# Performance work log

Hardware: AMD Instinct MI355X
Metric: run time of the kernel (lower is better)

Reference implementation:

```python
import jax, jax.numpy as jnp
import numpy as np

D_MODEL = 1024
N_HEADS = 16
D_K = D_MODEL // N_HEADS
B, T = 2, 2048
EPS = 1e-6


def _phi(x):
    # elu(x) + 1
    return jax.nn.elu(x) + 1.0


def setup_inputs() -> dict:
    key = jax.random.key(0)
    ks = jax.random.split(key, 5)
    s = 1.0 / np.sqrt(D_MODEL)
    return {
        "x": jax.random.normal(ks[0], (B, T, D_MODEL), jnp.float32),
        "Wq": jax.random.normal(ks[1], (D_MODEL, D_MODEL), jnp.float32) * s,
        "bq": jnp.zeros((D_MODEL,), jnp.float32),
        "Wk": jax.random.normal(ks[2], (D_MODEL, D_MODEL), jnp.float32) * s,
        "bk": jnp.zeros((D_MODEL,), jnp.float32),
        "Wv": jax.random.normal(ks[3], (D_MODEL, D_MODEL), jnp.float32) * s,
        "bv": jnp.zeros((D_MODEL,), jnp.float32),
        "Wo": jax.random.normal(ks[4], (D_MODEL, D_MODEL), jnp.float32) * s,
        "bo": jnp.zeros((D_MODEL,), jnp.float32),
    }


def reference(x, Wq, bq, Wk, bk, Wv, bv, Wo, bo):
    Bv_, Tv_, _ = x.shape
    # projections (torch nn.Linear: x @ W.T + b), split heads -> [B, H, T, d_k]
    def proj(W, b):
        y = x @ W.T + b
        return y.reshape(Bv_, Tv_, N_HEADS, D_K).transpose(0, 2, 1, 3)

    q = _phi(proj(Wq, bq))
    k = _phi(proj(Wk, bk))
    v = proj(Wv, bv)

    # causal linear attention: running kv outer-product and k prefix sums
    kv = jnp.einsum("bhtd,bhte->bhtde", k, v)          # [B,H,T,d_k,d_k]
    kv = jnp.cumsum(kv, axis=2)
    k_cum = jnp.cumsum(k, axis=2)
    out = jnp.einsum("bhtd,bhtde->bhte", q, kv)        # [B,H,T,d_k]
    z = jnp.einsum("bhtd,bhtd->bht", q, k_cum)         # [B,H,T]
    out = out / (z[..., None] + EPS)

    out = out.transpose(0, 2, 1, 3).reshape(Bv_, Tv_, N_HEADS * D_K)
    return out @ Wo.T + bo
```

## Files before the change

kernel.cpp:

```cpp
#include <hip/hip_runtime.h>


typedef float  f32x4   __attribute__((ext_vector_type(4)));
typedef __bf16 bf16x8  __attribute__((ext_vector_type(8)));
typedef short  short8v __attribute__((ext_vector_type(8)));
typedef short  short4v __attribute__((ext_vector_type(4)));

static __device__ __forceinline__ short f2bf(float f) {
    unsigned u = __float_as_uint(f);
    u += 0x7FFFu + ((u >> 16) & 1u);
    return (short)(u >> 16);
}
static __device__ __forceinline__ float bf2f(short s) {
    return __uint_as_float(((unsigned)(unsigned short)s) << 16);
}
static __device__ __forceinline__ float phi(float x) {
    return x > 0.f ? x + 1.f : __expf(x);
}
static __device__ __forceinline__ void gl_lds16(const short* g, short* l) {
    __builtin_amdgcn_global_load_lds(
        (const __attribute__((address_space(1))) void*)g,
        (__attribute__((address_space(3))) void*)l, 16, 0, 0);
}

#define LDT 72

__global__ __launch_bounds__(256) void convert_bf16(
    const float* __restrict__ x,  const float* __restrict__ Wq,
    const float* __restrict__ Wk, const float* __restrict__ Wv,
    const float* __restrict__ Wo,
    short* __restrict__ xb,  short* __restrict__ Wqb,
    short* __restrict__ Wkb, short* __restrict__ Wvb, short* __restrict__ Wob)
{
    const int blk = blockIdx.x;
    const float* src; short* dst; size_t base;
    if (blk < 2048)      { src = x;  dst = xb;  base = (size_t)blk * 2048; }
    else if (blk < 2560) { src = Wq; dst = Wqb; base = (size_t)(blk - 2048) * 2048; }
    else if (blk < 3072) { src = Wk; dst = Wkb; base = (size_t)(blk - 2560) * 2048; }
    else if (blk < 3584) { src = Wv; dst = Wvb; base = (size_t)(blk - 3072) * 2048; }
    else                 { src = Wo; dst = Wob; base = (size_t)(blk - 3584) * 2048; }
    const size_t o = base + (size_t)threadIdx.x * 8;
    f32x4 v0 = *(const f32x4*)&src[o];
    f32x4 v1 = *(const f32x4*)&src[o + 4];
    short8v s;
#pragma unroll
    for (int m = 0; m < 4; ++m) { s[m] = f2bf(v0[m]); s[m + 4] = f2bf(v1[m]); }
    *(short8v*)&dst[o] = s;
}

__global__ __launch_bounds__(256) void gemm_qkv(
    const short* __restrict__ xb,
    const short* __restrict__ Wqb, const short* __restrict__ Wkb,
    const short* __restrict__ Wvb,
    const float* __restrict__ bq, const float* __restrict__ bk,
    const float* __restrict__ bv,
    short* __restrict__ Qb, short* __restrict__ Kb, short* __restrict__ Vb)
{
    __shared__ short As[128 * 32];
    __shared__ short Bs[128 * 32];
    const int tid = threadIdx.x;
    const int bm = blockIdx.x, bn = blockIdx.y;
    const int wsel = bn >> 3;
    const int n0 = (bn & 7) << 7;
    const short* __restrict__ W    = (wsel == 0) ? Wqb : (wsel == 1) ? Wkb : Wvb;
    const float* __restrict__ bias = (wsel == 0) ? bq  : (wsel == 1) ? bk  : bv;
    short* __restrict__ Ob         = (wsel == 0) ? Qb  : (wsel == 1) ? Kb  : Vb;
    const int m0 = bm << 7;
    const int wave = tid >> 6, lane = tid & 63;
    const int wm = (wave & 1) << 6, wn = (wave >> 1) << 6;
    const int l15 = lane & 15, quad = lane >> 4;

    const int ch0 = wave * 2, ch1 = ch0 + 1;
    const int lrow = lane >> 2, lcol = (lane & 3) << 3;
    const short* ga0 = xb + (size_t)(m0 + ch0 * 16 + lrow) * 1024 + lcol;
    const short* ga1 = xb + (size_t)(m0 + ch1 * 16 + lrow) * 1024 + lcol;
    const short* gb0 = W  + (size_t)(n0 + ch0 * 16 + lrow) * 1024 + lcol;
    const short* gb1 = W  + (size_t)(n0 + ch1 * 16 + lrow) * 1024 + lcol;
    short* la0 = &As[ch0 * 512];
    short* la1 = &As[ch1 * 512];
    short* lb0 = &Bs[ch0 * 512];
    short* lb1 = &Bs[ch1 * 512];

    f32x4 acc[4][4] = {};
    for (int k0 = 0; k0 < 1024; k0 += 32) {
        __syncthreads();
        gl_lds16(ga0 + k0, la0);
        gl_lds16(ga1 + k0, la1);
        gl_lds16(gb0 + k0, lb0);
        gl_lds16(gb1 + k0, lb1);
        __syncthreads();
        bf16x8 a[4], b[4];
#pragma unroll
        for (int i = 0; i < 4; ++i) a[i] = *(const bf16x8*)&As[(wm + i * 16 + l15) * 32 + quad * 8];
#pragma unroll
        for (int j = 0; j < 4; ++j) b[j] = *(const bf16x8*)&Bs[(wn + j * 16 + l15) * 32 + quad * 8];
#pragma unroll
        for (int i = 0; i < 4; ++i)
#pragma unroll
            for (int j = 0; j < 4; ++j)
                acc[i][j] = __builtin_amdgcn_mfma_f32_16x16x32_bf16(a[i], b[j], acc[i][j], 0, 0, 0);
    }

#pragma unroll
    for (int i = 0; i < 4; ++i)
#pragma unroll
        for (int j = 0; j < 4; ++j) {
            const int col = n0 + wn + j * 16 + l15;
            const float bv_ = bias[col];
#pragma unroll
            for (int r = 0; r < 4; ++r) {
                const int row = m0 + wm + i * 16 + quad * 4 + r;
                float v = acc[i][j][r] + bv_;
                if (wsel < 2) v = phi(v);
                Ob[(size_t)row * 1024 + col] = f2bf(v);
            }
        }
}

__global__ __launch_bounds__(256) void chunk_sums(
    const short* __restrict__ Kb, const short* __restrict__ Vb,
    short* __restrict__ KVsum, float* __restrict__ ksum)
{
    __shared__ short KT[64 * LDT];
    __shared__ short VT[64 * LDT];
    __shared__ float pS[256];
    const int c = blockIdx.x, bh = blockIdx.y;
    const int b = bh >> 4, h = bh & 15;
    const int tid = threadIdx.x;
    const int w = tid >> 6, lane = tid & 63, l15 = lane & 15, quad = lane >> 4;
    const size_t rowbase = (size_t)b * 2048 + c * 64;

#pragma unroll
    for (int p = 0; p < 2; ++p) {
        const int t = (tid >> 3) + p * 32;
        const int e0 = (tid & 7) << 3;
        const size_t g = (rowbase + t) * 1024 + h * 64 + e0;
        short8v kv = *(const short8v*)&Kb[g];
        short8v vv = *(const short8v*)&Vb[g];
#pragma unroll
        for (int jj = 0; jj < 8; ++jj) {
            KT[(e0 + jj) * LDT + t] = kv[jj];
            VT[(e0 + jj) * LDT + t] = vv[jj];
        }
    }
    __syncthreads();

    f32x4 acc[4] = {};
#pragma unroll
    for (int k0 = 0; k0 < 64; k0 += 32) {
        bf16x8 a = *(const bf16x8*)&KT[(w * 16 + l15) * LDT + k0 + quad * 8];
#pragma unroll
        for (int tj = 0; tj < 4; ++tj) {
            bf16x8 bfr = *(const bf16x8*)&VT[(tj * 16 + l15) * LDT + k0 + quad * 8];
            acc[tj] = __builtin_amdgcn_mfma_f32_16x16x32_bf16(a, bfr, acc[tj], 0, 0, 0);
        }
    }
    short* __restrict__ outp = KVsum + (((size_t)bh * 32) + c) * 4096;
#pragma unroll
    for (int tj = 0; tj < 4; ++tj)
#pragma unroll
        for (int r = 0; r < 4; ++r)
            outp[(w * 16 + quad * 4 + r) * 64 + tj * 16 + l15] = f2bf(acc[tj][r]);

    {
        const int d = tid & 63, part = tid >> 6;
        short8v k1 = *(const short8v*)&KT[d * LDT + part * 16];
        short8v k2 = *(const short8v*)&KT[d * LDT + part * 16 + 8];
        float s = 0.f;
#pragma unroll
        for (int m = 0; m < 8; ++m) s += bf2f(k1[m]) + bf2f(k2[m]);
        pS[part * 64 + d] = s;
    }
    __syncthreads();
    if (tid < 64)
        ksum[(((size_t)bh * 32) + c) * 64 + tid] =
            pS[tid] + pS[tid + 64] + pS[tid + 128] + pS[tid + 192];
}

__global__ __launch_bounds__(256) void scan_chunks(
    const short* __restrict__ KVsum, const float* __restrict__ ksum,
    short* __restrict__ KVpref, float* __restrict__ kpref)
{
    const int bh = blockIdx.y;
    const int o = blockIdx.x * 256 + threadIdx.x;
    float run = 0.f;
    size_t base = (size_t)bh * 32 * 4096 + o;
    for (int cc = 0; cc < 32; ++cc) {
        KVpref[base] = f2bf(run);
        run += bf2f(KVsum[base]);
        base += 4096;
    }
    if (blockIdx.x == 0 && threadIdx.x < 64) {
        float vals[32];
        const size_t kb = (size_t)bh * 32 * 64 + threadIdx.x;
#pragma unroll
        for (int cc = 0; cc < 32; ++cc) vals[cc] = ksum[kb + (size_t)cc * 64];
        float r2 = 0.f;
#pragma unroll
        for (int cc = 0; cc < 32; ++cc) { kpref[kb + (size_t)cc * 64] = r2; r2 += vals[cc]; }
    }
}

__global__ __launch_bounds__(256) void attn_chunk(
    const short* __restrict__ Qb, const short* __restrict__ Kb,
    const short* __restrict__ Vb, const short* __restrict__ KVpref,
    const float* __restrict__ kpref, short* __restrict__ attnb)
{
    __shared__ short Qs[64 * LDT];
    __shared__ short KS[64 * LDT];
    __shared__ short VT[64 * LDT];
    __shared__ short KVT[64 * LDT];
    const int c = blockIdx.x, bh = blockIdx.y;
    const int b = bh >> 4, h = bh & 15;
    const int tid = threadIdx.x;
    const int w = tid >> 6, lane = tid & 63, l15 = lane & 15, quad = lane >> 4;
    const size_t rowbase = (size_t)b * 2048 + c * 64;
    const short* __restrict__ KVc = KVpref + (((size_t)bh * 32) + c) * 4096;

#pragma unroll
    for (int p = 0; p < 2; ++p) {
        const int t = (tid >> 3) + p * 32;
        const int e0 = (tid & 7) << 3;
        const size_t g = (rowbase + t) * 1024 + h * 64 + e0;
        *(short8v*)&Qs[t * LDT + e0] = *(const short8v*)&Qb[g];
        *(short8v*)&KS[t * LDT + e0] = *(const short8v*)&Kb[g];
        short8v vv = *(const short8v*)&Vb[g];
        short8v pv = *(const short8v*)&KVc[t * 64 + e0];
#pragma unroll
        for (int jj = 0; jj < 8; ++jj) {
            VT[(e0 + jj) * LDT + t]  = vv[jj];
            KVT[(e0 + jj) * LDT + t] = pv[jj];
        }
    }
    __syncthreads();

    f32x4 sacc[4] = {};
#pragma unroll
    for (int k0 = 0; k0 < 64; k0 += 32) {
        bf16x8 a = *(const bf16x8*)&Qs[(w * 16 + l15) * LDT + k0 + quad * 8];
#pragma unroll
        for (int tj = 0; tj < 4; ++tj) {
            bf16x8 bfr = *(const bf16x8*)&KS[(tj * 16 + l15) * LDT + k0 + quad * 8];
            sacc[tj] = __builtin_amdgcn_mfma_f32_16x16x32_bf16(a, bfr, sacc[tj], 0, 0, 0);
        }
    }

    f32x4 kp4 = *(const f32x4*)&kpref[(((size_t)bh * 32) + c) * 64 + l15 * 4];
    float zinv[4];
#pragma unroll
    for (int r = 0; r < 4; ++r) {
        const int i = w * 16 + quad * 4 + r;
        float p = 0.f;
#pragma unroll
        for (int tj = 0; tj < 4; ++tj)
            if (tj * 16 + l15 <= i) p += sacc[tj][r];
        short4v q4 = *(const short4v*)&Qs[i * LDT + l15 * 4];
#pragma unroll
        for (int m = 0; m < 4; ++m) p += bf2f(q4[m]) * kp4[m];
        p += __shfl_xor(p, 1);
        p += __shfl_xor(p, 2);
        p += __shfl_xor(p, 4);
        p += __shfl_xor(p, 8);
        zinv[r] = 1.f / (p + 1e-6f);
    }

    __syncthreads();
#pragma unroll
    for (int tj = 0; tj < 4; ++tj)
#pragma unroll
        for (int r = 0; r < 4; ++r) {
            const int i = w * 16 + quad * 4 + r;
            const int j = tj * 16 + l15;
            KS[i * LDT + j] = f2bf(j <= i ? sacc[tj][r] : 0.f);
        }
    __syncthreads();

    f32x4 oacc[4] = {};
#pragma unroll
    for (int k0 = 0; k0 < 64; k0 += 32) {
        bf16x8 a1 = *(const bf16x8*)&KS[(w * 16 + l15) * LDT + k0 + quad * 8];
        bf16x8 a2 = *(const bf16x8*)&Qs[(w * 16 + l15) * LDT + k0 + quad * 8];
#pragma unroll
        for (int tj = 0; tj < 4; ++tj) {
            bf16x8 b1 = *(const bf16x8*)&VT[(tj * 16 + l15) * LDT + k0 + quad * 8];
            bf16x8 b2 = *(const bf16x8*)&KVT[(tj * 16 + l15) * LDT + k0 + quad * 8];
            oacc[tj] = __builtin_amdgcn_mfma_f32_16x16x32_bf16(a1, b1, oacc[tj], 0, 0, 0);
            oacc[tj] = __builtin_amdgcn_mfma_f32_16x16x32_bf16(a2, b2, oacc[tj], 0, 0, 0);
        }
    }
#pragma unroll
    for (int tj = 0; tj < 4; ++tj)
#pragma unroll
        for (int r = 0; r < 4; ++r) {
            const int i = w * 16 + quad * 4 + r;
            const int e = tj * 16 + l15;
            attnb[(rowbase + i) * 1024 + h * 64 + e] = f2bf(oacc[tj][r] * zinv[r]);
        }
}

__global__ __launch_bounds__(256) void gemm_out(
    const short* __restrict__ attnb, const short* __restrict__ Wob,
    const float* __restrict__ bo, float* __restrict__ outp)
{
    __shared__ short As[128 * 32];
    __shared__ short Bs[128 * 32];
    const int tid = threadIdx.x;
    const int bm = blockIdx.x, bn = blockIdx.y;
    const int m0 = bm << 7, n0 = bn << 7;
    const int wave = tid >> 6, lane = tid & 63;
    const int wm = (wave & 1) << 6, wn = (wave >> 1) << 6;
    const int l15 = lane & 15, quad = lane >> 4;

    const int ch0 = wave * 2, ch1 = ch0 + 1;
    const int lrow = lane >> 2, lcol = (lane & 3) << 3;
    const short* ga0 = attnb + (size_t)(m0 + ch0 * 16 + lrow) * 1024 + lcol;
    const short* ga1 = attnb + (size_t)(m0 + ch1 * 16 + lrow) * 1024 + lcol;
    const short* gb0 = Wob   + (size_t)(n0 + ch0 * 16 + lrow) * 1024 + lcol;
    const short* gb1 = Wob   + (size_t)(n0 + ch1 * 16 + lrow) * 1024 + lcol;
    short* la0 = &As[ch0 * 512];
    short* la1 = &As[ch1 * 512];
    short* lb0 = &Bs[ch0 * 512];
    short* lb1 = &Bs[ch1 * 512];

    f32x4 acc[4][4] = {};
    for (int k0 = 0; k0 < 1024; k0 += 32) {
        __syncthreads();
        gl_lds16(ga0 + k0, la0);
        gl_lds16(ga1 + k0, la1);
        gl_lds16(gb0 + k0, lb0);
        gl_lds16(gb1 + k0, lb1);
        __syncthreads();
        bf16x8 a[4], b[4];
#pragma unroll
        for (int i = 0; i < 4; ++i) a[i] = *(const bf16x8*)&As[(wm + i * 16 + l15) * 32 + quad * 8];
#pragma unroll
        for (int j = 0; j < 4; ++j) b[j] = *(const bf16x8*)&Bs[(wn + j * 16 + l15) * 32 + quad * 8];
#pragma unroll
        for (int i = 0; i < 4; ++i)
#pragma unroll
            for (int j = 0; j < 4; ++j)
                acc[i][j] = __builtin_amdgcn_mfma_f32_16x16x32_bf16(a[i], b[j], acc[i][j], 0, 0, 0);
    }

#pragma unroll
    for (int i = 0; i < 4; ++i)
#pragma unroll
        for (int j = 0; j < 4; ++j) {
            const int col = n0 + wn + j * 16 + l15;
            const float bv_ = bo[col];
#pragma unroll
            for (int r = 0; r < 4; ++r) {
                const int row = m0 + wm + i * 16 + quad * 4 + r;
                outp[(size_t)row * 1024 + col] = acc[i][j][r] + bv_;
            }
        }
}

extern "C" void kernel_launch(void* const* d_in, const int* in_sizes, int n_in,
                              void* d_out, int out_size, void* d_ws, size_t ws_size,
                              hipStream_t stream)
{
    const float* x  = (const float*)d_in[0];
    const float* Wq = (const float*)d_in[1];
    const float* bq = (const float*)d_in[2];
    const float* Wk = (const float*)d_in[3];
    const float* bk = (const float*)d_in[4];
    const float* Wv = (const float*)d_in[5];
    const float* bv = (const float*)d_in[6];
    const float* Wo = (const float*)d_in[7];
    const float* bo = (const float*)d_in[8];

    char* ws = (char*)d_ws;
    short* xb     = (short*)(ws + 0);
    short* Wqb    = (short*)(ws + 8388608);
    short* Wkb    = (short*)(ws + 10485760);
    short* Wvb    = (short*)(ws + 12582912);
    short* Wob    = (short*)(ws + 14680064);
    short* Qb     = (short*)(ws + 16777216);
    short* Kb     = (short*)(ws + 25165824);
    short* Vb     = (short*)(ws + 33554432);
    short* KVsum  = (short*)(ws + 41943040);
    short* attnb  = (short*)(ws + 41943040);
    short* KVpref = (short*)(ws + 50331648);
    float* ksum   = (float*)(ws + 58720256);
    float* kpref  = (float*)(ws + 58982400);
    float* outp   = (float*)d_out;

    convert_bf16<<<4096, 256, 0, stream>>>(x, Wq, Wk, Wv, Wo, xb, Wqb, Wkb, Wvb, Wob);
    gemm_qkv   <<<dim3(32, 24), 256, 0, stream>>>(xb, Wqb, Wkb, Wvb, bq, bk, bv, Qb, Kb, Vb);
    chunk_sums <<<dim3(32, 32), 256, 0, stream>>>(Kb, Vb, KVsum, ksum);
    scan_chunks<<<dim3(16, 32), 256, 0, stream>>>(KVsum, ksum, KVpref, kpref);
    attn_chunk <<<dim3(32, 32), 256, 0, stream>>>(Qb, Kb, Vb, KVpref, kpref, attnb);
    gemm_out   <<<dim3(32, 8), 256, 0, stream>>>(attnb, Wob, bo, outp);
}
```

Measured before the change: 169.2 us.

## Fuse chunk prefix scan into attention kernel and shrink output GEMM N-tile

Removes the separate scan_chunks kernel. Each attention block now sums the preceding chunks' KV and k sums itself, in float registers, before writing the prefix into shared memory. This saves a kernel launch and the KVpref round trip through memory. In exchange, the redundant reads are quadratic in chunk index, so later chunks load up to 31 chunk-sums each. Separately, the output GEMM tile goes from 128x128 to 128x64, doubling the block count to 512 for better CU occupancy at the cost of more A-tile reloads.

```diff
diff --git a/kernel.cpp b/kernel.cpp
--- a/kernel.cpp
+++ b/kernel.cpp
@@ -177,59 +177,58 @@
             pS[tid] + pS[tid + 64] + pS[tid + 128] + pS[tid + 192];
 }
 
-__global__ __launch_bounds__(256) void scan_chunks(
-    const short* __restrict__ KVsum, const float* __restrict__ ksum,
-    short* __restrict__ KVpref, float* __restrict__ kpref)
-{
-    const int bh = blockIdx.y;
-    const int o = blockIdx.x * 256 + threadIdx.x;
-    float run = 0.f;
-    size_t base = (size_t)bh * 32 * 4096 + o;
-    for (int cc = 0; cc < 32; ++cc) {
-        KVpref[base] = f2bf(run);
-        run += bf2f(KVsum[base]);
-        base += 4096;
-    }
-    if (blockIdx.x == 0 && threadIdx.x < 64) {
-        float vals[32];
-        const size_t kb = (size_t)bh * 32 * 64 + threadIdx.x;
-#pragma unroll
-        for (int cc = 0; cc < 32; ++cc) vals[cc] = ksum[kb + (size_t)cc * 64];
-        float r2 = 0.f;
-#pragma unroll
-        for (int cc = 0; cc < 32; ++cc) { kpref[kb + (size_t)cc * 64] = r2; r2 += vals[cc]; }
-    }
-}
-
 __global__ __launch_bounds__(256) void attn_chunk(
     const short* __restrict__ Qb, const short* __restrict__ Kb,
-    const short* __restrict__ Vb, const short* __restrict__ KVpref,
-    const float* __restrict__ kpref, short* __restrict__ attnb)
+    const short* __restrict__ Vb, const short* __restrict__ KVsum,
+    const float* __restrict__ ksum, short* __restrict__ attnb)
 {
     __shared__ short Qs[64 * LDT];
     __shared__ short KS[64 * LDT];
     __shared__ short VT[64 * LDT];
     __shared__ short KVT[64 * LDT];
+    __shared__ float kp[64];
     const int c = blockIdx.x, bh = blockIdx.y;
     const int b = bh >> 4, h = bh & 15;
     const int tid = threadIdx.x;
     const int w = tid >> 6, lane = tid & 63, l15 = lane & 15, quad = lane >> 4;
     const size_t rowbase = (size_t)b * 2048 + c * 64;
-    const short* __restrict__ KVc = KVpref + (((size_t)bh * 32) + c) * 4096;
+
+    const int tA = tid >> 3;
+    const int e0 = (tid & 7) << 3;
+    float pref[16];
+#pragma unroll
+    for (int m = 0; m < 16; ++m) pref[m] = 0.f;
+    {
+        const short* __restrict__ Sb = KVsum + (size_t)bh * 32 * 4096;
+        for (int cc = 0; cc < c; ++cc) {
+            const short* __restrict__ S = Sb + cc * 4096;
+            short8v s0 = *(const short8v*)&S[tA * 64 + e0];
+            short8v s1 = *(const short8v*)&S[(tA + 32) * 64 + e0];
+#pragma unroll
+            for (int jj = 0; jj < 8; ++jj) {
+                pref[jj]     += bf2f(s0[jj]);
+                pref[8 + jj] += bf2f(s1[jj]);
+            }
+        }
+    }
+    if (tid < 64) {
+        float s = 0.f;
+        for (int cc = 0; cc < c; ++cc)
+            s += ksum[(((size_t)bh * 32) + cc) * 64 + tid];
+        kp[tid] = s;
+    }
 
 #pragma unroll
     for (int p = 0; p < 2; ++p) {
-        const int t = (tid >> 3) + p * 32;
-        const int e0 = (tid & 7) << 3;
+        const int t = tA + p * 32;
         const size_t g = (rowbase + t) * 1024 + h * 64 + e0;
         *(short8v*)&Qs[t * LDT + e0] = *(const short8v*)&Qb[g];
         *(short8v*)&KS[t * LDT + e0] = *(const short8v*)&Kb[g];
         short8v vv = *(const short8v*)&Vb[g];
-        short8v pv = *(const short8v*)&KVc[t * 64 + e0];
 #pragma unroll
         for (int jj = 0; jj < 8; ++jj) {
             VT[(e0 + jj) * LDT + t]  = vv[jj];
-            KVT[(e0 + jj) * LDT + t] = pv[jj];
+            KVT[(e0 + jj) * LDT + t] = f2bf(pref[p * 8 + jj]);
         }
     }
     __syncthreads();
@@ -245,7 +244,7 @@
         }
     }
 
-    f32x4 kp4 = *(const f32x4*)&kpref[(((size_t)bh * 32) + c) * 64 + l15 * 4];
+    f32x4 kp4 = *(const f32x4*)&kp[l15 * 4];
     float zinv[4];
 #pragma unroll
     for (int r = 0; r < 4; ++r) {
@@ -303,49 +302,51 @@
     const float* __restrict__ bo, float* __restrict__ outp)
 {
     __shared__ short As[128 * 32];
-    __shared__ short Bs[128 * 32];
+    __shared__ short Bs[64 * 32];
     const int tid = threadIdx.x;
     const int bm = blockIdx.x, bn = blockIdx.y;
-    const int m0 = bm << 7, n0 = bn << 7;
+    const int m0 = bm << 7, n0 = bn << 6;
     const int wave = tid >> 6, lane = tid & 63;
-    const int wm = (wave & 1) << 6, wn = (wave >> 1) << 6;
+    const int wm = (wave & 1) << 6, wn = (wave >> 1) << 5;
     const int l15 = lane & 15, quad = lane >> 4;
 
-    const int ch0 = wave * 2, ch1 = ch0 + 1;
     const int lrow = lane >> 2, lcol = (lane & 3) << 3;
-    const short* ga0 = attnb + (size_t)(m0 + ch0 * 16 + lrow) * 1024 + lcol;
-    const short* ga1 = attnb + (size_t)(m0 + ch1 * 16 + lrow) * 1024 + lcol;
-    const short* gb0 = Wob   + (size_t)(n0 + ch0 * 16 + lrow) * 1024 + lcol;
-    const short* gb1 = Wob   + (size_t)(n0 + ch1 * 16 + lrow) * 1024 + lcol;
-    short* la0 = &As[ch0 * 512];
-    short* la1 = &As[ch1 * 512];
-    short* lb0 = &Bs[ch0 * 512];
-    short* lb1 = &Bs[ch1 * 512];
-
-    f32x4 acc[4][4] = {};
+    const short* gp[3]; short* lp[3];
+#pragma unroll
+    for (int cc = 0; cc < 3; ++cc) {
+        const int ch = wave * 3 + cc;
+        if (ch < 8) {
+            gp[cc] = attnb + (size_t)(m0 + ch * 16 + lrow) * 1024 + lcol;
+            lp[cc] = &As[ch * 512];
+        } else {
+            gp[cc] = Wob + (size_t)(n0 + (ch - 8) * 16 + lrow) * 1024 + lcol;
+            lp[cc] = &Bs[(ch - 8) * 512];
+        }
+    }
+
+    f32x4 acc[4][2] = {};
     for (int k0 = 0; k0 < 1024; k0 += 32) {
         __syncthreads();
-        gl_lds16(ga0 + k0, la0);
-        gl_lds16(ga1 + k0, la1);
-        gl_lds16(gb0 + k0, lb0);
-        gl_lds16(gb1 + k0, lb1);
+        gl_lds16(gp[0] + k0, lp[0]);
+        gl_lds16(gp[1] + k0, lp[1]);
+        gl_lds16(gp[2] + k0, lp[2]);
         __syncthreads();
-        bf16x8 a[4], b[4];
+        bf16x8 a[4], b[2];
 #pragma unroll
         for (int i = 0; i < 4; ++i) a[i] = *(const bf16x8*)&As[(wm + i * 16 + l15) * 32 + quad * 8];
 #pragma unroll
-        for (int j = 0; j < 4; ++j) b[j] = *(const bf16x8*)&Bs[(wn + j * 16 + l15) * 32 + quad * 8];
+        for (int j = 0; j < 2; ++j) b[j] = *(const bf16x8*)&Bs[(wn + j * 16 + l15) * 32 + quad * 8];
 #pragma unroll
         for (int i = 0; i < 4; ++i)
 #pragma unroll
-            for (int j = 0; j < 4; ++j)
+            for (int j = 0; j < 2; ++j)
                 acc[i][j] = __builtin_amdgcn_mfma_f32_16x16x32_bf16(a[i], b[j], acc[i][j], 0, 0, 0);
     }
 
 #pragma unroll
     for (int i = 0; i < 4; ++i)
 #pragma unroll
-        for (int j = 0; j < 4; ++j) {
+        for (int j = 0; j < 2; ++j) {
             const int col = n0 + wn + j * 16 + l15;
             const float bv_ = bo[col];
 #pragma unroll
@@ -380,16 +381,13 @@
     short* Kb     = (short*)(ws + 25165824);
     short* Vb     = (short*)(ws + 33554432);
     short* KVsum  = (short*)(ws + 41943040);
-    short* attnb  = (short*)(ws + 41943040);
-    short* KVpref = (short*)(ws + 50331648);
+    short* attnb  = (short*)(ws + 50331648);
     float* ksum   = (float*)(ws + 58720256);
-    float* kpref  = (float*)(ws + 58982400);
     float* outp   = (float*)d_out;
 
     convert_bf16<<<4096, 256, 0, stream>>>(x, Wq, Wk, Wv, Wo, xb, Wqb, Wkb, Wvb, Wob);
     gemm_qkv   <<<dim3(32, 24), 256, 0, stream>>>(xb, Wqb, Wkb, Wvb, bq, bk, bv, Qb, Kb, Vb);
     chunk_sums <<<dim3(32, 32), 256, 0, stream>>>(Kb, Vb, KVsum, ksum);
-    scan_chunks<<<dim3(16, 32), 256, 0, stream>>>(KVsum, ksum, KVpref, kpref);
-    attn_chunk <<<dim3(32, 32), 256, 0, stream>>>(Qb, Kb, Vb, KVpref, kpref, attnb);
-    gemm_out   <<<dim3(32, 8), 256, 0, stream>>>(attnb, Wob, bo, outp);
-}
+    attn_chunk <<<dim3(32, 32), 256, 0, stream>>>(Qb, Kb, Vb, KVsum, ksum, attnb);
+    gemm_out   <<<dim3(32, 16), 256, 0, stream>>>(attnb, Wob, bo, outp);
+}
```

After: 173.6 us. +2.6%, slower.

## Write transposed K/V from QKV GEMM and fold chunk scan into attention

Applied to the files above, without the earlier changes.

The QKV GEMM epilogue now also writes K and V in a head-major, time-contiguous transposed layout. chunk_sums then loads MFMA operands straight from global memory, one wave per chunk, with no LDS transpose. The separate scan_chunks kernel is removed: each attention block sums the preceding chunk KV and k sums itself. This saves a launch and the prefix buffer round trip, at the cost of redundant prefix summation that grows with chunk index, plus an extra transposed K write.

```diff
diff --git a/kernel.cpp b/kernel.cpp
--- a/kernel.cpp
+++ b/kernel.cpp
@@ -54,7 +54,8 @@
     const short* __restrict__ Wvb,
     const float* __restrict__ bq, const float* __restrict__ bk,
     const float* __restrict__ bv,
-    short* __restrict__ Qb, short* __restrict__ Kb, short* __restrict__ Vb)
+    short* __restrict__ Qb, short* __restrict__ Kb,
+    short* __restrict__ Kt, short* __restrict__ Vt)
 {
     __shared__ short As[128 * 32];
     __shared__ short Bs[128 * 32];
@@ -64,7 +65,6 @@
     const int n0 = (bn & 7) << 7;
     const short* __restrict__ W    = (wsel == 0) ? Wqb : (wsel == 1) ? Wkb : Wvb;
     const float* __restrict__ bias = (wsel == 0) ? bq  : (wsel == 1) ? bk  : bv;
-    short* __restrict__ Ob         = (wsel == 0) ? Qb  : (wsel == 1) ? Kb  : Vb;
     const int m0 = bm << 7;
     const int wave = tid >> 6, lane = tid & 63;
     const int wm = (wave & 1) << 6, wn = (wave >> 1) << 6;
@@ -106,131 +106,144 @@
 #pragma unroll
         for (int j = 0; j < 4; ++j) {
             const int col = n0 + wn + j * 16 + l15;
+            const int h = col >> 6, d = col & 63;
             const float bv_ = bias[col];
-#pragma unroll
-            for (int r = 0; r < 4; ++r) {
-                const int row = m0 + wm + i * 16 + quad * 4 + r;
-                float v = acc[i][j][r] + bv_;
-                if (wsel < 2) v = phi(v);
-                Ob[(size_t)row * 1024 + col] = f2bf(v);
+            const int row0 = m0 + wm + i * 16 + quad * 4;
+            const int b = row0 >> 11, t0 = row0 & 2047;
+            const size_t tbase = ((size_t)(b * 16 + h) * 64 + d) * 2048 + t0;
+            if (wsel == 2) {
+                short4v s4;
+#pragma unroll
+                for (int r = 0; r < 4; ++r) s4[r] = f2bf(acc[i][j][r] + bv_);
+                *(short4v*)&Vt[tbase] = s4;
+            } else if (wsel == 1) {
+                short4v s4;
+#pragma unroll
+                for (int r = 0; r < 4; ++r) {
+                    const float v = phi(acc[i][j][r] + bv_);
+                    const short sv = f2bf(v);
+                    s4[r] = sv;
+                    Kb[(size_t)(row0 + r) * 1024 + col] = sv;
+                }
+                *(short4v*)&Kt[tbase] = s4;
+            } else {
+#pragma unroll
+                for (int r = 0; r < 4; ++r)
+                    Qb[(size_t)(row0 + r) * 1024 + col] = f2bf(phi(acc[i][j][r] + bv_));
             }
         }
 }
 
 __global__ __launch_bounds__(256) void chunk_sums(
-    const short* __restrict__ Kb, const short* __restrict__ Vb,
-    short* __restrict__ KVsum, float* __restrict__ ksum)
-{
-    __shared__ short KT[64 * LDT];
+    const short* __restrict__ Kt, const short* __restrict__ Vt,
+    short* __restrict__ KVsumT, float* __restrict__ ksum)
+{
+    const int tid = threadIdx.x;
+    const int wave = tid >> 6, lane = tid & 63;
+    const int l15 = lane & 15, quad = lane >> 4;
+    const int c = blockIdx.x * 4 + wave;
+    const int bh = blockIdx.y;
+    const short* __restrict__ KtB = Kt + (size_t)bh * 64 * 2048;
+    const short* __restrict__ VtB = Vt + (size_t)bh * 64 * 2048;
+    const int tb = c * 64 + quad * 8;
+
+    bf16x8 ak[4][2], bv[4][2];
+#pragma unroll
+    for (int da = 0; da < 4; ++da)
+#pragma unroll
+        for (int k0 = 0; k0 < 2; ++k0) {
+            ak[da][k0] = *(const bf16x8*)&KtB[(size_t)(da * 16 + l15) * 2048 + tb + k0 * 32];
+            bv[da][k0] = *(const bf16x8*)&VtB[(size_t)(da * 16 + l15) * 2048 + tb + k0 * 32];
+        }
+
+    f32x4 acc[4][4] = {};
+#pragma unroll
+    for (int da = 0; da < 4; ++da)
+#pragma unroll
+        for (int ea = 0; ea < 4; ++ea)
+#pragma unroll
+            for (int k0 = 0; k0 < 2; ++k0)
+                acc[da][ea] = __builtin_amdgcn_mfma_f32_16x16x32_bf16(
+                    ak[da][k0], bv[ea][k0], acc[da][ea], 0, 0, 0);
+
+    short* __restrict__ outp = KVsumT + ((size_t)bh * 32 + c) * 4096;
+#pragma unroll
+    for (int da = 0; da < 4; ++da)
+#pragma unroll
+        for (int ea = 0; ea < 4; ++ea) {
+            short4v s4;
+#pragma unroll
+            for (int r = 0; r < 4; ++r) s4[r] = f2bf(acc[da][ea][r]);
+            *(short4v*)&outp[(ea * 16 + l15) * 64 + da * 16 + quad * 4] = s4;
+        }
+
+#pragma unroll
+    for (int da = 0; da < 4; ++da) {
+        float s = 0.f;
+#pragma unroll
+        for (int k0 = 0; k0 < 2; ++k0)
+#pragma unroll
+            for (int m = 0; m < 8; ++m) s += (float)ak[da][k0][m];
+        s += __shfl_xor(s, 16);
+        s += __shfl_xor(s, 32);
+        if (lane < 16)
+            ksum[((size_t)bh * 32 + c) * 64 + da * 16 + l15] = s;
+    }
+}
+
+__global__ __launch_bounds__(256) void attn_chunk(
+    const short* __restrict__ Qb, const short* __restrict__ Kb,
+    const short* __restrict__ Vt, const short* __restrict__ KVsumT,
+    const float* __restrict__ ksum, short* __restrict__ attnb)
+{
+    __shared__ short Qs[64 * LDT];
+    __shared__ short KS[64 * LDT];
     __shared__ short VT[64 * LDT];
-    __shared__ float pS[256];
+    __shared__ short KVT[64 * LDT];
+    __shared__ float kp[64];
     const int c = blockIdx.x, bh = blockIdx.y;
     const int b = bh >> 4, h = bh & 15;
     const int tid = threadIdx.x;
     const int w = tid >> 6, lane = tid & 63, l15 = lane & 15, quad = lane >> 4;
     const size_t rowbase = (size_t)b * 2048 + c * 64;
 
+    const int tA = tid >> 3;
+    const int e0 = (tid & 7) << 3;
+    float pref[16];
+#pragma unroll
+    for (int m = 0; m < 16; ++m) pref[m] = 0.f;
+    {
+        const short* __restrict__ Sb = KVsumT + (size_t)bh * 32 * 4096;
+        for (int cc = 0; cc < c; ++cc) {
+            const short* __restrict__ S = Sb + cc * 4096;
+            short8v s0 = *(const short8v*)&S[tA * 64 + e0];
+            short8v s1 = *(const short8v*)&S[(tA + 32) * 64 + e0];
+#pragma unroll
+            for (int jj = 0; jj < 8; ++jj) {
+                pref[jj]     += bf2f(s0[jj]);
+                pref[8 + jj] += bf2f(s1[jj]);
+            }
+        }
+    }
+    if (tid < 64) {
+        float s = 0.f;
+        for (int cc = 0; cc < c; ++cc)
+            s += ksum[((size_t)bh * 32 + cc) * 64 + tid];
+        kp[tid] = s;
+    }
+
 #pragma unroll
     for (int p = 0; p < 2; ++p) {
-        const int t = (tid >> 3) + p * 32;
-        const int e0 = (tid & 7) << 3;
-        const size_t g = (rowbase + t) * 1024 + h * 64 + e0;
-        short8v kv = *(const short8v*)&Kb[g];
-        short8v vv = *(const short8v*)&Vb[g];
-#pragma unroll
-        for (int jj = 0; jj < 8; ++jj) {
-            KT[(e0 + jj) * LDT + t] = kv[jj];
-            VT[(e0 + jj) * LDT + t] = vv[jj];
-        }
-    }
-    __syncthreads();
-
-    f32x4 acc[4] = {};
-#pragma unroll
-    for (int k0 = 0; k0 < 64; k0 += 32) {
-        bf16x8 a = *(const bf16x8*)&KT[(w * 16 + l15) * LDT + k0 + quad * 8];
-#pragma unroll
-        for (int tj = 0; tj < 4; ++tj) {
-            bf16x8 bfr = *(const bf16x8*)&VT[(tj * 16 + l15) * LDT + k0 + quad * 8];
-            acc[tj] = __builtin_amdgcn_mfma_f32_16x16x32_bf16(a, bfr, acc[tj], 0, 0, 0);
-        }
-    }
-    short* __restrict__ outp = KVsum + (((size_t)bh * 32) + c) * 4096;
-#pragma unroll
-    for (int tj = 0; tj < 4; ++tj)
-#pragma unroll
-        for (int r = 0; r < 4; ++r)
-            outp[(w * 16 + quad * 4 + r) * 64 + tj * 16 + l15] = f2bf(acc[tj][r]);
-
-    {
-        const int d = tid & 63, part = tid >> 6;
-        short8v k1 = *(const short8v*)&KT[d * LDT + part * 16];
-        short8v k2 = *(const short8v*)&KT[d * LDT + part * 16 + 8];
-        float s = 0.f;
-#pragma unroll
-        for (int m = 0; m < 8; ++m) s += bf2f(k1[m]) + bf2f(k2[m]);
-        pS[part * 64 + d] = s;
-    }
-    __syncthreads();
-    if (tid < 64)
-        ksum[(((size_t)bh * 32) + c) * 64 + tid] =
-            pS[tid] + pS[tid + 64] + pS[tid + 128] + pS[tid + 192];
-}
-
-__global__ __launch_bounds__(256) void scan_chunks(
-    const short* __restrict__ KVsum, const float* __restrict__ ksum,
-    short* __restrict__ KVpref, float* __restrict__ kpref)
-{
-    const int bh = blockIdx.y;
-    const int o = blockIdx.x * 256 + threadIdx.x;
-    float run = 0.f;
-    size_t base = (size_t)bh * 32 * 4096 + o;
-    for (int cc = 0; cc < 32; ++cc) {
-        KVpref[base] = f2bf(run);
-        run += bf2f(KVsum[base]);
-        base += 4096;
-    }
-    if (blockIdx.x == 0 && threadIdx.x < 64) {
-        float vals[32];
-        const size_t kb = (size_t)bh * 32 * 64 + threadIdx.x;
-#pragma unroll
-        for (int cc = 0; cc < 32; ++cc) vals[cc] = ksum[kb + (size_t)cc * 64];
-        float r2 = 0.f;
-#pragma unroll
-        for (int cc = 0; cc < 32; ++cc) { kpref[kb + (size_t)cc * 64] = r2; r2 += vals[cc]; }
-    }
-}
-
-__global__ __launch_bounds__(256) void attn_chunk(
-    const short* __restrict__ Qb, const short* __restrict__ Kb,
-    const short* __restrict__ Vb, const short* __restrict__ KVpref,
-    const float* __restrict__ kpref, short* __restrict__ attnb)
-{
-    __shared__ short Qs[64 * LDT];
-    __shared__ short KS[64 * LDT];
-    __shared__ short VT[64 * LDT];
-    __shared__ short KVT[64 * LDT];
-    const int c = blockIdx.x, bh = blockIdx.y;
-    const int b = bh >> 4, h = bh & 15;
-    const int tid = threadIdx.x;
-    const int w = tid >> 6, lane = tid & 63, l15 = lane & 15, quad = lane >> 4;
-    const size_t rowbase = (size_t)b * 2048 + c * 64;
-    const short* __restrict__ KVc = KVpref + (((size_t)bh * 32) + c) * 4096;
-
-#pragma unroll
-    for (int p = 0; p < 2; ++p) {
-        const int t = (tid >> 3) + p * 32;
-        const int e0 = (tid & 7) << 3;
+        const int t = tA + p * 32;
         const size_t g = (rowbase + t) * 1024 + h * 64 + e0;
         *(short8v*)&Qs[t * LDT + e0] = *(const short8v*)&Qb[g];
         *(short8v*)&KS[t * LDT + e0] = *(const short8v*)&Kb[g];
-        short8v vv = *(const short8v*)&Vb[g];
-        short8v pv = *(const short8v*)&KVc[t * 64 + e0];
-#pragma unroll
-        for (int jj = 0; jj < 8; ++jj) {
-            VT[(e0 + jj) * LDT + t]  = vv[jj];
-            KVT[(e0 + jj) * LDT + t] = pv[jj];
-        }
+        *(short8v*)&VT[t * LDT + e0] =
+            *(const short8v*)&Vt[((size_t)bh * 64 + t) * 2048 + c * 64 + e0];
+        short8v pv;
+#pragma unroll
+        for (int jj = 0; jj < 8; ++jj) pv[jj] = f2bf(pref[p * 8 + jj]);
+        *(short8v*)&KVT[t * LDT + e0] = pv;
     }
     __syncthreads();
 
@@ -245,7 +258,7 @@
         }
     }
 
-    f32x4 kp4 = *(const f32x4*)&kpref[(((size_t)bh * 32) + c) * 64 + l15 * 4];
+    f32x4 kp4 = *(const f32x4*)&kp[l15 * 4];
     float zinv[4];
 #pragma unroll
     for (int r = 0; r < 4; ++r) {
@@ -371,25 +384,23 @@
     const float* bo = (const float*)d_in[8];
 
     char* ws = (char*)d_ws;
-    short* xb     = (short*)(ws + 0);
-    short* Wqb    = (short*)(ws + 8388608);
-    short* Wkb    = (short*)(ws + 10485760);
-    short* Wvb    = (short*)(ws + 12582912);
-    short* Wob    = (short*)(ws + 14680064);
-    short* Qb     = (short*)(ws + 16777216);
-    short* Kb     = (short*)(ws + 25165824);
-    short* Vb     = (short*)(ws + 33554432);
-    short* KVsum  = (short*)(ws + 41943040);
-    short* attnb  = (short*)(ws + 41943040);
-    short* KVpref = (short*)(ws + 50331648);
-    float* ksum   = (float*)(ws + 58720256);
-    float* kpref  = (float*)(ws + 58982400);
-    float* outp   = (float*)d_out;
+    short* xb      = (short*)(ws + 0);
+    short* Wqb     = (short*)(ws + 8388608);
+    short* Wkb     = (short*)(ws + 10485760);
+    short* Wvb     = (short*)(ws + 12582912);
+    short* Wob     = (short*)(ws + 14680064);
+    short* Qb      = (short*)(ws + 16777216);
+    short* Kb      = (short*)(ws + 25165824);
+    short* Kt      = (short*)(ws + 33554432);
+    short* Vt      = (short*)(ws + 41943040);
+    short* KVsumT  = (short*)(ws + 50331648);
+    short* attnb   = (short*)(ws + 58720256);
+    float* ksum    = (float*)(ws + 67108864);
+    float* outp    = (float*)d_out;
 
     convert_bf16<<<4096, 256, 0, stream>>>(x, Wq, Wk, Wv, Wo, xb, Wqb, Wkb, Wvb, Wob);
-    gemm_qkv   <<<dim3(32, 24), 256, 0, stream>>>(xb, Wqb, Wkb, Wvb, bq, bk, bv, Qb, Kb, Vb);
-    chunk_sums <<<dim3(32, 32), 256, 0, stream>>>(Kb, Vb, KVsum, ksum);
-    scan_chunks<<<dim3(16, 32), 256, 0, stream>>>(KVsum, ksum, KVpref, kpref);
-    attn_chunk <<<dim3(32, 32), 256, 0, stream>>>(Qb, Kb, Vb, KVpref, kpref, attnb);
+    gemm_qkv   <<<dim3(32, 24), 256, 0, stream>>>(xb, Wqb, Wkb, Wvb, bq, bk, bv, Qb, Kb, Kt, Vt);
+    chunk_sums <<<dim3(8, 32), 256, 0, stream>>>(Kt, Vt, KVsumT, ksum);
+    attn_chunk <<<dim3(32, 32), 256, 0, stream>>>(Qb, Kb, Vt, KVsumT, ksum, attnb);
     gemm_out   <<<dim3(32, 8), 256, 0, stream>>>(attnb, Wob, bo, outp);
 }
```

Result: slower. 191.2 us (+13.0%).
